# Performance work log

Hardware: AMD Instinct MI355X
Metric: run time of the kernel (lower is better)

## Reference

```python
import jax, jax.numpy as jnp
import numpy as np

NEG_SLOPE = 0.2  # PyG GATConv default LeakyReLU slope


def gat_layer(x, src, dst, W, a_src, a_dst, bias, num_nodes, heads, out_ch, concat):
    # x: [N, in], W: [in, heads*out_ch], a_src/a_dst: [heads, out_ch]
    h = (x @ W).reshape(num_nodes, heads, out_ch)          # [N,H,C]
    alpha_s = jnp.sum(h * a_src, axis=-1)                  # [N,H]
    alpha_d = jnp.sum(h * a_dst, axis=-1)                  # [N,H]
    e = jax.nn.leaky_relu(alpha_s[src] + alpha_d[dst], NEG_SLOPE)  # [E,H]
    # softmax over incoming edges of each destination node
    e_max = jax.ops.segment_max(e, dst, num_segments=num_nodes)   # [N,H]
    e_exp = jnp.exp(e - e_max[dst])                        # [E,H]
    denom = jax.ops.segment_sum(e_exp, dst, num_segments=num_nodes)  # [N,H]
    alpha = e_exp / denom[dst]                             # [E,H]
    msg = h[src] * alpha[:, :, None]                       # [E,H,C]
    out = jax.ops.segment_sum(msg, dst, num_segments=num_nodes)     # [N,H,C]
    if concat:
        out = out.reshape(num_nodes, heads * out_ch)
    else:
        out = out.mean(axis=1)
    return out + bias


def setup_inputs() -> dict:
    key = jax.random.key(0)
    ks = jax.random.split(key, 12)
    N, E = 50000, 800000
    IN, HID, OUT, H = 128, 32, 64, 4
    x = jax.random.normal(ks[0], (N, IN), dtype=jnp.float32)
    edge_index = jax.random.randint(ks[1], (2, E), 0, N, dtype=jnp.int32)
    s = 1.0 / np.sqrt(IN)
    W1 = jax.random.normal(ks[2], (IN, H * HID), dtype=jnp.float32) * s
    a_src1 = jax.random.normal(ks[3], (H, HID), dtype=jnp.float32) * 0.1
    a_dst1 = jax.random.normal(ks[4], (H, HID), dtype=jnp.float32) * 0.1
    b1 = jnp.zeros((H * HID,), dtype=jnp.float32)
    s2 = 1.0 / np.sqrt(H * HID)
    W2 = jax.random.normal(ks[5], (H * HID, OUT), dtype=jnp.float32) * s2
    a_src2 = jax.random.normal(ks[6], (1, OUT), dtype=jnp.float32) * 0.1
    a_dst2 = jax.random.normal(ks[7], (1, OUT), dtype=jnp.float32) * 0.1
    b2 = jnp.zeros((OUT,), dtype=jnp.float32)
    return {"x": x, "edge_index": edge_index, "W1": W1, "a_src1": a_src1,
            "a_dst1": a_dst1, "b1": b1, "W2": W2, "a_src2": a_src2,
            "a_dst2": a_dst2, "b2": b2}


def reference(x, edge_index, W1, a_src1, a_dst1, b1, W2, a_src2, a_dst2, b2):
    N = x.shape[0]
    src, dst = edge_index[0], edge_index[1]
    h = gat_layer(x, src, dst, W1, a_src1, a_dst1, b1, N, heads=4, out_ch=32, concat=True)
    h = jax.nn.elu(h)
    # dropout is identity in eval / p=0.0
    out = gat_layer(h, src, dst, W2, a_src2, a_dst2, b2, N, heads=1, out_ch=64, concat=False)
    return out
```

## Files before the change

### kernel.cpp

```cpp
#include <hip/hip_runtime.h>

#define C1 128
#define C2 64
#define CAP 96

typedef __attribute__((ext_vector_type(8))) _Float16 half8;
typedef __attribute__((ext_vector_type(2))) _Float16 half2v;
typedef __attribute__((ext_vector_type(2))) __fp16  fp16x2;
typedef __attribute__((ext_vector_type(4))) float floatx4;

__device__ __forceinline__ float lrelu(float v) { return v > 0.f ? v : 0.2f * v; }

__device__ __forceinline__ unsigned short f2h(float f) {
    union { _Float16 h; unsigned short u; } c;
    c.h = (_Float16)f;
    return c.u;
}
__device__ __forceinline__ unsigned pk2h(float a, float b) {
    union { fp16x2 p; unsigned u; } c;
    c.p = __builtin_amdgcn_cvt_pkrtz(a, b);
    return c.u;
}

__global__ __launch_bounds__(256)
void gemm1_mfma_kernel(const float* __restrict__ x, const float* __restrict__ W1,
                       const float* __restrict__ asrc, const float* __restrict__ adst,
                       unsigned short* __restrict__ h1b,
                       float* __restrict__ as1, float* __restrict__ ad1,
                       int N) {
    __shared__ __align__(16) unsigned short Bs[128 * 136];
    for (int i = threadIdx.x; i < 128 * 64; i += 256) {
        int col = i & 127;
        int k = (i >> 7) * 2;
        *(unsigned*)&Bs[col * 136 + k] = pk2h(W1[k * 128 + col], W1[(k + 1) * 128 + col]);
    }
    __syncthreads();

    const int lane = threadIdx.x & 63, ww = threadIdx.x >> 6;
    const int quad = lane >> 4, l16 = lane & 15;
    const int nodeBase = blockIdx.x * 64 + ww * 16;
    int arow = nodeBase + l16;
    if (arow >= N) arow = N - 1;
    const float* xp = x + (size_t)arow * C1 + quad * 8;
    half8 afr[4];
#pragma unroll
    for (int kk = 0; kk < 4; ++kk) {
        float4 a0 = *(const float4*)(xp + kk * 32);
        float4 a1 = *(const float4*)(xp + kk * 32 + 4);
        union { half8 v; unsigned u[4]; } fr;
        fr.u[0] = pk2h(a0.x, a0.y);
        fr.u[1] = pk2h(a0.z, a0.w);
        fr.u[2] = pk2h(a1.x, a1.y);
        fr.u[3] = pk2h(a1.z, a1.w);
        afr[kk] = fr.v;
    }

    float sacc[4], dacc[4];
#pragma unroll
    for (int ct = 0; ct < 8; ++ct) {
        floatx4 acc = {0.f, 0.f, 0.f, 0.f};
        const int col = ct * 16 + l16;
        const unsigned short* bbase = &Bs[col * 136 + quad * 8];
#pragma unroll
        for (int kk = 0; kk < 4; ++kk) {
            half8 bfr = *(const half8*)(bbase + kk * 32);
            acc = __builtin_amdgcn_mfma_f32_16x16x32_f16(afr[kk], bfr, acc, 0, 0, 0);
        }
#pragma unroll
        for (int reg = 0; reg < 4; ++reg) {
            int node = nodeBase + quad * 4 + reg;
            if (node < N) h1b[(size_t)node * C1 + col] = f2h(acc[reg]);
        }
        float av = asrc[col];
        float dv = adst[col];
        if ((ct & 1) == 0) {
#pragma unroll
            for (int r = 0; r < 4; ++r) { sacc[r] = 0.f; dacc[r] = 0.f; }
        }
#pragma unroll
        for (int reg = 0; reg < 4; ++reg) {
            sacc[reg] += acc[reg] * av;
            dacc[reg] += acc[reg] * dv;
        }
        if ((ct & 1) == 1) {
            int h = ct >> 1;
#pragma unroll
            for (int reg = 0; reg < 4; ++reg) {
                float ts = sacc[reg], td = dacc[reg];
#pragma unroll
                for (int o = 1; o < 16; o <<= 1) {
                    ts += __shfl_xor(ts, o, 64);
                    td += __shfl_xor(td, o, 64);
                }
                if (l16 == 0) {
                    int node = nodeBase + quad * 4 + reg;
                    if (node < N) {
                        as1[node * 4 + h] = ts;
                        ad1[node * 4 + h] = td;
                    }
                }
            }
        }
    }
}

__global__ __launch_bounds__(256)
void fill_kernel(const int* __restrict__ ei, int* __restrict__ cursor,
                 int* __restrict__ csrc, int N, int E) {
    const int part = blockIdx.x & 7;
    const int bIdx = blockIdx.x >> 3;
    const int bpp  = gridDim.x >> 3;
    const int lo = (int)(((long)N * part) >> 3);
    const int hi = (int)(((long)N * (part + 1)) >> 3);

    const int E4 = ((E & 3) == 0) ? (E >> 2) : 0;
    const int4* d4 = (const int4*)(ei + E);
    const int4* s4 = (const int4*)ei;
    for (int q = bIdx * 256 + threadIdx.x; q < E4; q += bpp * 256) {
        int4 dv = d4[q];
        int4 sv = s4[q];
        int dd[4] = {dv.x, dv.y, dv.z, dv.w};
        int ss[4] = {sv.x, sv.y, sv.z, sv.w};
        int pos[4];
        bool act[4];
#pragma unroll
        for (int i = 0; i < 4; ++i) {
            act[i] = (dd[i] >= lo) & (dd[i] < hi) & ((unsigned)ss[i] < (unsigned)N);
            pos[i] = act[i] ? atomicAdd(&cursor[dd[i]], 1) : 0;
        }
#pragma unroll
        for (int i = 0; i < 4; ++i)
            if (act[i] && pos[i] < CAP) csrc[dd[i] * CAP + pos[i]] = ss[i];
    }
    for (int e = E4 * 4 + bIdx * 256 + threadIdx.x; e < E; e += bpp * 256) {
        int dd = ei[E + e];
        if (dd < lo || dd >= hi) continue;
        int ss = ei[e];
        if ((unsigned)ss >= (unsigned)N) continue;
        int pp = atomicAdd(&cursor[dd], 1);
        if (pp < CAP) csrc[dd * CAP + pp] = ss;
    }
}

__global__ __launch_bounds__(256)
void msg1_csr_kernel(const int* __restrict__ cursor, const int* __restrict__ csrc,
                     const unsigned* __restrict__ h1u, const float* __restrict__ as1,
                     const float* __restrict__ ad1, const float* __restrict__ b1,
                     unsigned* __restrict__ out1, int N) {
    __shared__ float ws[4][64];
    const int wid = threadIdx.x >> 6;
    const int d = blockIdx.x * 4 + wid;
    if (d >= N) return;
    const int lane = threadIdx.x & 63;
    int dg = cursor[d]; if (dg > CAP) dg = CAP;
    const int base = d * CAP;
    const int e16 = lane & 15;
    const int head = lane >> 4;
    const float wadh = ad1[d * 4 + head];
    float accx = 0.f, accy = 0.f, sumw = 0.f;
    for (int jj = 0; jj < dg; jj += 16) {
        int idx = jj + e16;
        if (idx >= dg) idx = dg - 1;
        const int myS = csrc[base + idx];
        unsigned rv[16];
#pragma unroll
        for (int k = 0; k < 16; ++k) {
            int s = __builtin_amdgcn_readlane(myS, k);
            rv[k] = h1u[(unsigned)s * 64u + (unsigned)lane];
        }
        float w = 0.f;
        if (jj + e16 < dg)
            w = __expf(lrelu(as1[myS * 4 + head] + wadh));
        ws[wid][lane] = w;
#pragma unroll
        for (int j = 0; j < 4; ++j) {
            float4 wf = ((const float4*)&ws[wid][head * 16])[j];
            union { unsigned u; half2v p; } c0, c1, c2, c3;
            c0.u = rv[4 * j + 0]; c1.u = rv[4 * j + 1];
            c2.u = rv[4 * j + 2]; c3.u = rv[4 * j + 3];
            sumw += (wf.x + wf.y) + (wf.z + wf.w);
            accx += wf.x * (float)c0.p[0]; accy += wf.x * (float)c0.p[1];
            accx += wf.y * (float)c1.p[0]; accy += wf.y * (float)c1.p[1];
            accx += wf.z * (float)c2.p[0]; accy += wf.z * (float)c2.p[1];
            accx += wf.w * (float)c3.p[0]; accy += wf.w * (float)c3.p[1];
        }
    }
    float inv = (sumw > 0.f) ? 1.f / sumw : 0.f;
    float rx = accx * inv + b1[2 * lane];
    float ry = accy * inv + b1[2 * lane + 1];
    rx = rx > 0.f ? rx : expm1f(rx);
    ry = ry > 0.f ? ry : expm1f(ry);
    out1[(size_t)d * 64 + lane] = pk2h(rx, ry);
}

__global__ __launch_bounds__(256)
void gemm2_mfma_kernel(const unsigned short* __restrict__ h2, const float* __restrict__ W2,
                       const float* __restrict__ asrc, const float* __restrict__ adst,
                       unsigned short* __restrict__ g2b, float* __restrict__ as2,
                       float* __restrict__ ad2, int N) {
    __shared__ __align__(16) unsigned short Bs[64 * 136];
    for (int i = threadIdx.x; i < 64 * 64; i += 256) {
        int col = i & 63;
        int k = (i >> 6) * 2;
        *(unsigned*)&Bs[col * 136 + k] = pk2h(W2[k * 64 + col], W2[(k + 1) * 64 + col]);
    }
    __syncthreads();

    const int lane = threadIdx.x & 63, ww = threadIdx.x >> 6;
    const int quad = lane >> 4, l16 = lane & 15;
    const int nodeBase = blockIdx.x * 64 + ww * 16;
    int arow = nodeBase + l16;
    if (arow >= N) arow = N - 1;
    const unsigned short* xp = h2 + (size_t)arow * C1 + quad * 8;
    half8 afr[4];
#pragma unroll
    for (int kk = 0; kk < 4; ++kk)
        afr[kk] = *(const half8*)(xp + kk * 32);

    float sacc[4] = {0.f,0.f,0.f,0.f}, dacc[4] = {0.f,0.f,0.f,0.f};
#pragma unroll
    for (int ct = 0; ct < 4; ++ct) {
        floatx4 acc = {0.f, 0.f, 0.f, 0.f};
        const int col = ct * 16 + l16;
        const unsigned short* bbase = &Bs[col * 136 + quad * 8];
#pragma unroll
        for (int kk = 0; kk < 4; ++kk) {
            half8 bfr = *(const half8*)(bbase + kk * 32);
            acc = __builtin_amdgcn_mfma_f32_16x16x32_f16(afr[kk], bfr, acc, 0, 0, 0);
        }
#pragma unroll
        for (int reg = 0; reg < 4; ++reg) {
            int node = nodeBase + quad * 4 + reg;
            if (node < N) g2b[(size_t)node * C2 + col] = f2h(acc[reg]);
        }
        float av = asrc[col];
        float dv = adst[col];
#pragma unroll
        for (int reg = 0; reg < 4; ++reg) {
            sacc[reg] += acc[reg] * av;
            dacc[reg] += acc[reg] * dv;
        }
    }
#pragma unroll
    for (int reg = 0; reg < 4; ++reg) {
        float ts = sacc[reg], td = dacc[reg];
#pragma unroll
        for (int o = 1; o < 16; o <<= 1) {
            ts += __shfl_xor(ts, o, 64);
            td += __shfl_xor(td, o, 64);
        }
        if (l16 == 0) {
            int node = nodeBase + quad * 4 + reg;
            if (node < N) { as2[node] = ts; ad2[node] = td; }
        }
    }
}

__global__ __launch_bounds__(256)
void msg2_csr_kernel(const int* __restrict__ cursor, const int* __restrict__ csrc,
                     const unsigned* __restrict__ g2u, const float* __restrict__ as2,
                     const float* __restrict__ ad2, const float* __restrict__ b2,
                     float2* __restrict__ y, int N) {
    __shared__ float wsm[4][32];
    __shared__ int   ssm[4][32];
    const int wid = threadIdx.x >> 6;
    const int d = blockIdx.x * 4 + wid;
    if (d >= N) return;
    const int lane = threadIdx.x & 63;
    const int half = lane >> 5;
    const int l32 = lane & 31;
    int dg = cursor[d]; if (dg > CAP) dg = CAP;
    const int base = d * CAP;
    const float add = ad2[d];
    float accx = 0.f, accy = 0.f, sumw = 0.f;
    for (int jj = 0; jj < dg; jj += 32) {
        int idx = jj + l32;
        if (idx >= dg) idx = dg - 1;
        const int myS = csrc[base + idx];
        float w = 0.f;
        if (jj + l32 < dg) w = __expf(lrelu(as2[myS] + add));
        ssm[wid][l32] = myS;
        wsm[wid][l32] = w;
        int4 s0 = ((const int4*)&ssm[wid][half * 16])[0];
        int4 s1 = ((const int4*)&ssm[wid][half * 16])[1];
        int4 s2 = ((const int4*)&ssm[wid][half * 16])[2];
        int4 s3 = ((const int4*)&ssm[wid][half * 16])[3];
        int ss[16] = {s0.x, s0.y, s0.z, s0.w, s1.x, s1.y, s1.z, s1.w,
                      s2.x, s2.y, s2.z, s2.w, s3.x, s3.y, s3.z, s3.w};
        unsigned rv[16];
#pragma unroll
        for (int k = 0; k < 16; ++k)
            rv[k] = g2u[(unsigned)ss[k] * 32u + (unsigned)l32];
#pragma unroll
        for (int j = 0; j < 4; ++j) {
            float4 wf = ((const float4*)&wsm[wid][half * 16])[j];
            union { unsigned u; half2v p; } c0, c1, c2, c3;
            c0.u = rv[4 * j + 0]; c1.u = rv[4 * j + 1];
            c2.u = rv[4 * j + 2]; c3.u = rv[4 * j + 3];
            sumw += (wf.x + wf.y) + (wf.z + wf.w);
            accx += wf.x * (float)c0.p[0]; accy += wf.x * (float)c0.p[1];
            accx += wf.y * (float)c1.p[0]; accy += wf.y * (float)c1.p[1];
            accx += wf.z * (float)c2.p[0]; accy += wf.z * (float)c2.p[1];
            accx += wf.w * (float)c3.p[0]; accy += wf.w * (float)c3.p[1];
        }
    }
    accx += __shfl_xor(accx, 32, 64);
    accy += __shfl_xor(accy, 32, 64);
    sumw += __shfl_xor(sumw, 32, 64);
    if (half == 0) {
        float inv = (sumw > 0.f) ? 1.f / sumw : 0.f;
        float2 p;
        p.x = accx * inv + b2[2 * l32];
        p.y = accy * inv + b2[2 * l32 + 1];
        y[(size_t)d * 32 + l32] = p;
    }
}

extern "C" void kernel_launch(void* const* d_in, const int* in_sizes, int n_in,
                              void* d_out, int out_size, void* d_ws, size_t ws_size,
                              hipStream_t stream) {
    const float* x    = (const float*)d_in[0];
    const int*   ei   = (const int*)d_in[1];
    const float* W1   = (const float*)d_in[2];
    const float* a_s1 = (const float*)d_in[3];
    const float* a_d1 = (const float*)d_in[4];
    const float* b1   = (const float*)d_in[5];
    const float* W2   = (const float*)d_in[6];
    const float* a_s2 = (const float*)d_in[7];
    const float* a_d2 = (const float*)d_in[8];
    const float* b2   = (const float*)d_in[9];

    const int N = in_sizes[0] / C1;
    const int E = in_sizes[1] / 2;

    auto align16 = [](size_t v) { return (v + 15) & ~(size_t)15; };
    const size_t RF   = 16;
    const size_t RCUR = align16((size_t)N * 4);
    const size_t RSRC = align16((size_t)N * CAP * 4);
    const size_t R1   = align16((size_t)N * C1 * 4);
    const size_t R2   = align16((size_t)N * 8 * 4);

    char* base = (char*)d_ws;
    int*  cursor = (int*)(base + RF);
    int*  csrc   = (int*)(base + RF + RCUR);
    char* R1p = base + RF + RCUR + RSRC;
    char* R2p = R1p + R1;
    char* R4p = R2p + R2;
    (void)ws_size;

    unsigned short* h1 = (unsigned short*)R1p;
    unsigned short* g2 = (unsigned short*)R1p;
    float* as1 = (float*)R2p;
    float* ad1 = as1 + (size_t)N * 4;
    float* as2 = (float*)R2p;
    float* ad2 = as2 + N;
    unsigned short* out1 = (unsigned short*)R4p;

    const int nbTile = (N + 63) / 64;
    const int nbWave4 = (N + 3) / 4;

    hipMemsetAsync(cursor, 0, (size_t)N * 4, stream);
    gemm1_mfma_kernel<<<nbTile, 256, 0, stream>>>(x, W1, a_s1, a_d1, h1, as1, ad1, N);
    fill_kernel<<<2048, 256, 0, stream>>>(ei, cursor, csrc, N, E);
    msg1_csr_kernel<<<nbWave4, 256, 0, stream>>>(cursor, csrc, (const unsigned*)h1,
        as1, ad1, b1, (unsigned*)out1, N);
    gemm2_mfma_kernel<<<nbTile, 256, 0, stream>>>(out1, W2, a_s2, a_d2, g2, as2, ad2, N);
    msg2_csr_kernel<<<nbWave4, 256, 0, stream>>>(cursor, csrc, (const unsigned*)g2,
        as2, ad2, b2, (float2*)d_out, N);
}
```

Measured before the change: 226.1 us.

## Permute fp16 feature layout to pair MFMA tiles and use persistent message kernels

The GEMM kernels now compute two 16-column MFMA tiles together and store them as packed half2 words (col, col+16 within a head for layer 1; col, col+32 for layer 2). That replaces scattered 16-bit stores with 32-bit stores and fuses the attention-score reduction per head without the separate accumulate phase. The gemm2 weight staging and bias indexing in the message kernels are permuted to match the new interleaved layout, and the final output is written as two strided floats. Both message kernels become grid-stride loops over destinations with a fixed 2048-block grid instead of one wave per node, which reduces block launch overhead but may lower load balance.

Result: slower. 237.7 us (+5.1%).

```diff
diff --git a/kernel.cpp b/kernel.cpp
--- a/kernel.cpp
+++ b/kernel.cpp
@@ -25,7 +25,7 @@
 __global__ __launch_bounds__(256)
 void gemm1_mfma_kernel(const float* __restrict__ x, const float* __restrict__ W1,
                        const float* __restrict__ asrc, const float* __restrict__ adst,
-                       unsigned short* __restrict__ h1b,
+                       unsigned* __restrict__ h1d,
                        float* __restrict__ as1, float* __restrict__ ad1,
                        int N) {
     __shared__ __align__(16) unsigned short Bs[128 * 136];
@@ -55,49 +55,42 @@
         afr[kk] = fr.v;
     }
 
-    float sacc[4], dacc[4];
-#pragma unroll
-    for (int ct = 0; ct < 8; ++ct) {
-        floatx4 acc = {0.f, 0.f, 0.f, 0.f};
-        const int col = ct * 16 + l16;
-        const unsigned short* bbase = &Bs[col * 136 + quad * 8];
+#pragma unroll
+    for (int h = 0; h < 4; ++h) {
+        floatx4 accL = {0.f, 0.f, 0.f, 0.f};
+        floatx4 accH = {0.f, 0.f, 0.f, 0.f};
+        const int colL = h * 32 + l16;
+        const int colH = colL + 16;
+        const unsigned short* bL = &Bs[colL * 136 + quad * 8];
+        const unsigned short* bH = &Bs[colH * 136 + quad * 8];
 #pragma unroll
         for (int kk = 0; kk < 4; ++kk) {
-            half8 bfr = *(const half8*)(bbase + kk * 32);
-            acc = __builtin_amdgcn_mfma_f32_16x16x32_f16(afr[kk], bfr, acc, 0, 0, 0);
+            half8 bfrL = *(const half8*)(bL + kk * 32);
+            half8 bfrH = *(const half8*)(bH + kk * 32);
+            accL = __builtin_amdgcn_mfma_f32_16x16x32_f16(afr[kk], bfrL, accL, 0, 0, 0);
+            accH = __builtin_amdgcn_mfma_f32_16x16x32_f16(afr[kk], bfrH, accH, 0, 0, 0);
         }
 #pragma unroll
         for (int reg = 0; reg < 4; ++reg) {
             int node = nodeBase + quad * 4 + reg;
-            if (node < N) h1b[(size_t)node * C1 + col] = f2h(acc[reg]);
-        }
-        float av = asrc[col];
-        float dv = adst[col];
-        if ((ct & 1) == 0) {
-#pragma unroll
-            for (int r = 0; r < 4; ++r) { sacc[r] = 0.f; dacc[r] = 0.f; }
-        }
+            if (node < N) h1d[(size_t)node * 64 + h * 16 + l16] = pk2h(accL[reg], accH[reg]);
+        }
+        float avL = asrc[colL], dvL = adst[colL];
+        float avH = asrc[colH], dvH = adst[colH];
 #pragma unroll
         for (int reg = 0; reg < 4; ++reg) {
-            sacc[reg] += acc[reg] * av;
-            dacc[reg] += acc[reg] * dv;
-        }
-        if ((ct & 1) == 1) {
-            int h = ct >> 1;
-#pragma unroll
-            for (int reg = 0; reg < 4; ++reg) {
-                float ts = sacc[reg], td = dacc[reg];
-#pragma unroll
-                for (int o = 1; o < 16; o <<= 1) {
-                    ts += __shfl_xor(ts, o, 64);
-                    td += __shfl_xor(td, o, 64);
-                }
-                if (l16 == 0) {
-                    int node = nodeBase + quad * 4 + reg;
-                    if (node < N) {
-                        as1[node * 4 + h] = ts;
-                        ad1[node * 4 + h] = td;
-                    }
+            float ts = accL[reg] * avL + accH[reg] * avH;
+            float td = accL[reg] * dvL + accH[reg] * dvH;
+#pragma unroll
+            for (int o = 1; o < 16; o <<= 1) {
+                ts += __shfl_xor(ts, o, 64);
+                td += __shfl_xor(td, o, 64);
+            }
+            if (l16 == 0) {
+                int node = nodeBase + quad * 4 + reg;
+                if (node < N) {
+                    as1[node * 4 + h] = ts;
+                    ad1[node * 4 + h] = td;
                 }
             }
         }
@@ -149,60 +142,65 @@
                      unsigned* __restrict__ out1, int N) {
     __shared__ float ws[4][64];
     const int wid = threadIdx.x >> 6;
-    const int d = blockIdx.x * 4 + wid;
-    if (d >= N) return;
     const int lane = threadIdx.x & 63;
-    int dg = cursor[d]; if (dg > CAP) dg = CAP;
-    const int base = d * CAP;
     const int e16 = lane & 15;
     const int head = lane >> 4;
-    const float wadh = ad1[d * 4 + head];
-    float accx = 0.f, accy = 0.f, sumw = 0.f;
-    for (int jj = 0; jj < dg; jj += 16) {
-        int idx = jj + e16;
-        if (idx >= dg) idx = dg - 1;
-        const int myS = csrc[base + idx];
-        unsigned rv[16];
-#pragma unroll
-        for (int k = 0; k < 16; ++k) {
-            int s = __builtin_amdgcn_readlane(myS, k);
-            rv[k] = h1u[(unsigned)s * 64u + (unsigned)lane];
-        }
-        float w = 0.f;
-        if (jj + e16 < dg)
-            w = __expf(lrelu(as1[myS * 4 + head] + wadh));
-        ws[wid][lane] = w;
-#pragma unroll
-        for (int j = 0; j < 4; ++j) {
-            float4 wf = ((const float4*)&ws[wid][head * 16])[j];
-            union { unsigned u; half2v p; } c0, c1, c2, c3;
-            c0.u = rv[4 * j + 0]; c1.u = rv[4 * j + 1];
-            c2.u = rv[4 * j + 2]; c3.u = rv[4 * j + 3];
-            sumw += (wf.x + wf.y) + (wf.z + wf.w);
-            accx += wf.x * (float)c0.p[0]; accy += wf.x * (float)c0.p[1];
-            accx += wf.y * (float)c1.p[0]; accy += wf.y * (float)c1.p[1];
-            accx += wf.z * (float)c2.p[0]; accy += wf.z * (float)c2.p[1];
-            accx += wf.w * (float)c3.p[0]; accy += wf.w * (float)c3.p[1];
-        }
-    }
-    float inv = (sumw > 0.f) ? 1.f / sumw : 0.f;
-    float rx = accx * inv + b1[2 * lane];
-    float ry = accy * inv + b1[2 * lane + 1];
-    rx = rx > 0.f ? rx : expm1f(rx);
-    ry = ry > 0.f ? ry : expm1f(ry);
-    out1[(size_t)d * 64 + lane] = pk2h(rx, ry);
+    const float bx = b1[32 * head + e16];
+    const float by = b1[32 * head + e16 + 16];
+    const int dstride = gridDim.x << 2;
+
+    for (int d = blockIdx.x * 4 + wid; d < N; d += dstride) {
+        int dg = cursor[d]; if (dg > CAP) dg = CAP;
+        const int base = d * CAP;
+        const float wadh = ad1[d * 4 + head];
+        float accx = 0.f, accy = 0.f, sumw = 0.f;
+        for (int jj = 0; jj < dg; jj += 16) {
+            int idx = jj + e16;
+            if (idx >= dg) idx = dg - 1;
+            const int myS = csrc[base + idx];
+            unsigned rv[16];
+#pragma unroll
+            for (int k = 0; k < 16; ++k) {
+                int s = __builtin_amdgcn_readlane(myS, k);
+                rv[k] = h1u[(unsigned)s * 64u + (unsigned)lane];
+            }
+            float w = 0.f;
+            if (jj + e16 < dg)
+                w = __expf(lrelu(as1[myS * 4 + head] + wadh));
+            ws[wid][lane] = w;
+#pragma unroll
+            for (int j = 0; j < 4; ++j) {
+                float4 wf = ((const float4*)&ws[wid][head * 16])[j];
+                union { unsigned u; half2v p; } c0, c1, c2, c3;
+                c0.u = rv[4 * j + 0]; c1.u = rv[4 * j + 1];
+                c2.u = rv[4 * j + 2]; c3.u = rv[4 * j + 3];
+                sumw += (wf.x + wf.y) + (wf.z + wf.w);
+                accx += wf.x * (float)c0.p[0]; accy += wf.x * (float)c0.p[1];
+                accx += wf.y * (float)c1.p[0]; accy += wf.y * (float)c1.p[1];
+                accx += wf.z * (float)c2.p[0]; accy += wf.z * (float)c2.p[1];
+                accx += wf.w * (float)c3.p[0]; accy += wf.w * (float)c3.p[1];
+            }
+        }
+        float inv = (sumw > 0.f) ? 1.f / sumw : 0.f;
+        float rx = accx * inv + bx;
+        float ry = accy * inv + by;
+        rx = rx > 0.f ? rx : expm1f(rx);
+        ry = ry > 0.f ? ry : expm1f(ry);
+        out1[(size_t)d * 64 + lane] = pk2h(rx, ry);
+    }
 }
 
 __global__ __launch_bounds__(256)
 void gemm2_mfma_kernel(const unsigned short* __restrict__ h2, const float* __restrict__ W2,
                        const float* __restrict__ asrc, const float* __restrict__ adst,
-                       unsigned short* __restrict__ g2b, float* __restrict__ as2,
+                       unsigned* __restrict__ g2d, float* __restrict__ as2,
                        float* __restrict__ ad2, int N) {
     __shared__ __align__(16) unsigned short Bs[64 * 136];
     for (int i = threadIdx.x; i < 64 * 64; i += 256) {
         int col = i & 63;
-        int k = (i >> 6) * 2;
-        *(unsigned*)&Bs[col * 136 + k] = pk2h(W2[k * 64 + col], W2[(k + 1) * 64 + col]);
+        int p = i >> 6;
+        int k0 = 32 * (p >> 4) + (p & 15);
+        *(unsigned*)&Bs[col * 136 + 2 * p] = pk2h(W2[k0 * 64 + col], W2[(k0 + 16) * 64 + col]);
     }
     __syncthreads();
 
@@ -219,26 +217,31 @@
 
     float sacc[4] = {0.f,0.f,0.f,0.f}, dacc[4] = {0.f,0.f,0.f,0.f};
 #pragma unroll
-    for (int ct = 0; ct < 4; ++ct) {
-        floatx4 acc = {0.f, 0.f, 0.f, 0.f};
-        const int col = ct * 16 + l16;
-        const unsigned short* bbase = &Bs[col * 136 + quad * 8];
+    for (int ctp = 0; ctp < 2; ++ctp) {
+        floatx4 accL = {0.f, 0.f, 0.f, 0.f};
+        floatx4 accH = {0.f, 0.f, 0.f, 0.f};
+        const int colL = ctp * 16 + l16;
+        const int colH = colL + 32;
+        const unsigned short* bL = &Bs[colL * 136 + quad * 8];
+        const unsigned short* bH = &Bs[colH * 136 + quad * 8];
 #pragma unroll
         for (int kk = 0; kk < 4; ++kk) {
-            half8 bfr = *(const half8*)(bbase + kk * 32);
-            acc = __builtin_amdgcn_mfma_f32_16x16x32_f16(afr[kk], bfr, acc, 0, 0, 0);
+            half8 bfrL = *(const half8*)(bL + kk * 32);
+            half8 bfrH = *(const half8*)(bH + kk * 32);
+            accL = __builtin_amdgcn_mfma_f32_16x16x32_f16(afr[kk], bfrL, accL, 0, 0, 0);
+            accH = __builtin_amdgcn_mfma_f32_16x16x32_f16(afr[kk], bfrH, accH, 0, 0, 0);
         }
 #pragma unroll
         for (int reg = 0; reg < 4; ++reg) {
             int node = nodeBase + quad * 4 + reg;
-            if (node < N) g2b[(size_t)node * C2 + col] = f2h(acc[reg]);
-        }
-        float av = asrc[col];
-        float dv = adst[col];
+            if (node < N) g2d[(size_t)node * 32 + colL] = pk2h(accL[reg], accH[reg]);
+        }
+        float avL = asrc[colL], dvL = adst[colL];
+        float avH = asrc[colH], dvH = adst[colH];
 #pragma unroll
         for (int reg = 0; reg < 4; ++reg) {
-            sacc[reg] += acc[reg] * av;
-            dacc[reg] += acc[reg] * dv;
+            sacc[reg] += accL[reg] * avL + accH[reg] * avH;
+            dacc[reg] += accL[reg] * dvL + accH[reg] * dvH;
         }
     }
 #pragma unroll
@@ -260,59 +263,61 @@
 void msg2_csr_kernel(const int* __restrict__ cursor, const int* __restrict__ csrc,
                      const unsigned* __restrict__ g2u, const float* __restrict__ as2,
                      const float* __restrict__ ad2, const float* __restrict__ b2,
-                     float2* __restrict__ y, int N) {
+                     float* __restrict__ yf, int N) {
     __shared__ float wsm[4][32];
     __shared__ int   ssm[4][32];
     const int wid = threadIdx.x >> 6;
-    const int d = blockIdx.x * 4 + wid;
-    if (d >= N) return;
     const int lane = threadIdx.x & 63;
     const int half = lane >> 5;
     const int l32 = lane & 31;
-    int dg = cursor[d]; if (dg > CAP) dg = CAP;
-    const int base = d * CAP;
-    const float add = ad2[d];
-    float accx = 0.f, accy = 0.f, sumw = 0.f;
-    for (int jj = 0; jj < dg; jj += 32) {
-        int idx = jj + l32;
-        if (idx >= dg) idx = dg - 1;
-        const int myS = csrc[base + idx];
-        float w = 0.f;
-        if (jj + l32 < dg) w = __expf(lrelu(as2[myS] + add));
-        ssm[wid][l32] = myS;
-        wsm[wid][l32] = w;
-        int4 s0 = ((const int4*)&ssm[wid][half * 16])[0];
-        int4 s1 = ((const int4*)&ssm[wid][half * 16])[1];
-        int4 s2 = ((const int4*)&ssm[wid][half * 16])[2];
-        int4 s3 = ((const int4*)&ssm[wid][half * 16])[3];
-        int ss[16] = {s0.x, s0.y, s0.z, s0.w, s1.x, s1.y, s1.z, s1.w,
-                      s2.x, s2.y, s2.z, s2.w, s3.x, s3.y, s3.z, s3.w};
-        unsigned rv[16];
-#pragma unroll
-        for (int k = 0; k < 16; ++k)
-            rv[k] = g2u[(unsigned)ss[k] * 32u + (unsigned)l32];
-#pragma unroll
-        for (int j = 0; j < 4; ++j) {
-            float4 wf = ((const float4*)&wsm[wid][half * 16])[j];
-            union { unsigned u; half2v p; } c0, c1, c2, c3;
-            c0.u = rv[4 * j + 0]; c1.u = rv[4 * j + 1];
-            c2.u = rv[4 * j + 2]; c3.u = rv[4 * j + 3];
-            sumw += (wf.x + wf.y) + (wf.z + wf.w);
-            accx += wf.x * (float)c0.p[0]; accy += wf.x * (float)c0.p[1];
-            accx += wf.y * (float)c1.p[0]; accy += wf.y * (float)c1.p[1];
-            accx += wf.z * (float)c2.p[0]; accy += wf.z * (float)c2.p[1];
-            accx += wf.w * (float)c3.p[0]; accy += wf.w * (float)c3.p[1];
-        }
-    }
-    accx += __shfl_xor(accx, 32, 64);
-    accy += __shfl_xor(accy, 32, 64);
-    sumw += __shfl_xor(sumw, 32, 64);
-    if (half == 0) {
-        float inv = (sumw > 0.f) ? 1.f / sumw : 0.f;
-        float2 p;
-        p.x = accx * inv + b2[2 * l32];
-        p.y = accy * inv + b2[2 * l32 + 1];
-        y[(size_t)d * 32 + l32] = p;
+    const float bx = b2[l32];
+    const float by = b2[l32 + 32];
+    const int dstride = gridDim.x << 2;
+
+    for (int d = blockIdx.x * 4 + wid; d < N; d += dstride) {
+        int dg = cursor[d]; if (dg > CAP) dg = CAP;
+        const int base = d * CAP;
+        const float add = ad2[d];
+        float accx = 0.f, accy = 0.f, sumw = 0.f;
+        for (int jj = 0; jj < dg; jj += 32) {
+            int idx = jj + l32;
+            if (idx >= dg) idx = dg - 1;
+            const int myS = csrc[base + idx];
+            float w = 0.f;
+            if (jj + l32 < dg) w = __expf(lrelu(as2[myS] + add));
+            ssm[wid][l32] = myS;
+            wsm[wid][l32] = w;
+            int4 s0 = ((const int4*)&ssm[wid][half * 16])[0];
+            int4 s1 = ((const int4*)&ssm[wid][half * 16])[1];
+            int4 s2 = ((const int4*)&ssm[wid][half * 16])[2];
+            int4 s3 = ((const int4*)&ssm[wid][half * 16])[3];
+            int ss[16] = {s0.x, s0.y, s0.z, s0.w, s1.x, s1.y, s1.z, s1.w,
+                          s2.x, s2.y, s2.z, s2.w, s3.x, s3.y, s3.z, s3.w};
+            unsigned rv[16];
+#pragma unroll
+            for (int k = 0; k < 16; ++k)
+                rv[k] = g2u[(unsigned)ss[k] * 32u + (unsigned)l32];
+#pragma unroll
+            for (int j = 0; j < 4; ++j) {
+                float4 wf = ((const float4*)&wsm[wid][half * 16])[j];
+                union { unsigned u; half2v p; } c0, c1, c2, c3;
+                c0.u = rv[4 * j + 0]; c1.u = rv[4 * j + 1];
+                c2.u = rv[4 * j + 2]; c3.u = rv[4 * j + 3];
+                sumw += (wf.x + wf.y) + (wf.z + wf.w);
+                accx += wf.x * (float)c0.p[0]; accy += wf.x * (float)c0.p[1];
+                accx += wf.y * (float)c1.p[0]; accy += wf.y * (float)c1.p[1];
+                accx += wf.z * (float)c2.p[0]; accy += wf.z * (float)c2.p[1];
+                accx += wf.w * (float)c3.p[0]; accy += wf.w * (float)c3.p[1];
+            }
+        }
+        accx += __shfl_xor(accx, 32, 64);
+        accy += __shfl_xor(accy, 32, 64);
+        sumw += __shfl_xor(sumw, 32, 64);
+        if (half == 0) {
+            float inv = (sumw > 0.f) ? 1.f / sumw : 0.f;
+            yf[(size_t)d * 64 + l32]      = accx * inv + bx;
+            yf[(size_t)d * 64 + 32 + l32] = accy * inv + by;
+        }
     }
 }
 
@@ -348,23 +353,23 @@
     char* R4p = R2p + R2;
     (void)ws_size;
 
-    unsigned short* h1 = (unsigned short*)R1p;
-    unsigned short* g2 = (unsigned short*)R1p;
+    unsigned* h1 = (unsigned*)R1p;
+    unsigned* g2 = (unsigned*)R1p;
     float* as1 = (float*)R2p;
     float* ad1 = as1 + (size_t)N * 4;
     float* as2 = (float*)R2p;
     float* ad2 = as2 + N;
-    unsigned short* out1 = (unsigned short*)R4p;
+    unsigned* out1 = (unsigned*)R4p;
 
     const int nbTile = (N + 63) / 64;
-    const int nbWave4 = (N + 3) / 4;
 
     hipMemsetAsync(cursor, 0, (size_t)N * 4, stream);
     gemm1_mfma_kernel<<<nbTile, 256, 0, stream>>>(x, W1, a_s1, a_d1, h1, as1, ad1, N);
     fill_kernel<<<2048, 256, 0, stream>>>(ei, cursor, csrc, N, E);
-    msg1_csr_kernel<<<nbWave4, 256, 0, stream>>>(cursor, csrc, (const unsigned*)h1,
-        as1, ad1, b1, (unsigned*)out1, N);
-    gemm2_mfma_kernel<<<nbTile, 256, 0, stream>>>(out1, W2, a_s2, a_d2, g2, as2, ad2, N);
-    msg2_csr_kernel<<<nbWave4, 256, 0, stream>>>(cursor, csrc, (const unsigned*)g2,
-        as2, ad2, b2, (float2*)d_out, N);
-}
+    msg1_csr_kernel<<<2048, 256, 0, stream>>>(cursor, csrc, (const unsigned*)h1,
+        as1, ad1, b1, out1, N);
+    gemm2_mfma_kernel<<<nbTile, 256, 0, stream>>>((const unsigned short*)out1, W2,
+        a_s2, a_d2, g2, as2, ad2, N);
+    msg2_csr_kernel<<<2048, 256, 0, stream>>>(cursor, csrc, (const unsigned*)g2,
+        as2, ad2, b2, (float*)d_out, N);
+}
```
